# Performance work log

Hardware: AMD Instinct MI355X
Metric: run time of the kernel (lower is better)

## Reference

```python
import jax, jax.numpy as jnp
import numpy as np

N_USER = 60000
N_ITEM = 40000
N = N_USER + N_ITEM          # total nodes
D = 64                        # embed_size
E_HALF = 400000               # undirected interactions; E = 2*E_HALF symmetric directed edges
N_LAYERS = 3                  # len(args.layer_size)
BETA = 0.5                    # self.beta_
EPS = 1e-8                    # torch cosine_similarity eps


def setup_inputs() -> dict:
    key = jax.random.key(0)
    ks = jax.random.split(key, 8)
    # symmetric bipartite edge list: (u, n_user+i) and its reverse
    u = jax.random.randint(ks[0], (E_HALF,), 0, N_USER)
    it = jax.random.randint(ks[1], (E_HALF,), 0, N_ITEM) + N_USER
    src = jnp.concatenate([u, it])
    dst = jnp.concatenate([it, u])
    # rev_perm[e] gives the index of edge (dst[e], src[e])
    rev_perm = jnp.concatenate([jnp.arange(E_HALF) + E_HALF, jnp.arange(E_HALF)])
    vals_half = jax.random.uniform(ks[2], (E_HALF,), minval=0.01, maxval=0.1)
    adj_vals = jnp.concatenate([vals_half, vals_half])  # symmetric normalized adjacency values
    user_emb = 0.1 * jax.random.normal(ks[3], (N_USER, D), dtype=jnp.float32)
    item_emb = 0.1 * jax.random.normal(ks[4], (N_ITEM, D), dtype=jnp.float32)
    W_prune = jax.random.normal(ks[5], (1, 2), dtype=jnp.float32) / jnp.sqrt(2.0)
    b_prune = jnp.zeros((1,), dtype=jnp.float32)
    users = jax.random.randint(ks[6], (2048,), 0, N_USER)
    items = jax.random.randint(ks[7], (2048,), 0, N_ITEM)
    return {"users": users, "items": items, "user_emb": user_emb, "item_emb": item_emb,
            "W_prune": W_prune, "b_prune": b_prune, "src": src, "dst": dst,
            "rev_perm": rev_perm, "adj_vals": adj_vals}


def _computer(user_emb, item_emb, W_prune, b_prune, adj_vals, src, dst, rev_perm):
    emb = jnp.concatenate([user_emb, item_emb], axis=0)  # [N, D]
    embs = [emb]
    mem = adj_vals                                        # memory = adj values at start
    for _ in range(N_LAYERS):
        es, ed = emb[src], emb[dst]                       # [E, D] edge gathers
        # per-edge cosine similarity (torch eps clamp on denominator)
        num = jnp.sum(es * ed, axis=-1)
        den = jnp.maximum(jnp.linalg.norm(es, axis=-1) * jnp.linalg.norm(ed, axis=-1), EPS)
        cos = num / den
        # row-wise L1 normalization over adjacency nonzeros (sklearn normalize, norm='l1')
        rowsum = jax.ops.segment_sum(jnp.abs(cos), src, num_segments=N)
        denom = rowsum[src]
        coef = cos / jnp.where(denom > 0, denom, 1.0)
        # pruning: Linear(2,1) on [coef[r,c], coef[c,r]], sigmoid, keep iff > 0.5
        cv = jnp.stack([coef, coef[rev_perm]], axis=-1)   # [E, 2]
        p = jax.nn.sigmoid(cv @ W_prune.T + b_prune)[:, 0]
        decision = (p > 0.5).astype(coef.dtype)
        coef = coef * decision
        # memory EMA, then elementwise multiply with adjacency -> propagation weights
        mem = BETA * mem + (1.0 - BETA) * coef
        g = mem * adj_vals
        # sparse matmul: out[r] = sum_c A[r,c] * emb[c]
        emb = jax.ops.segment_sum(g[:, None] * ed, src, num_segments=N)
        embs.append(emb)
    light_out = jnp.mean(jnp.stack(embs, axis=1), axis=1)  # [N, D]
    return light_out[:N_USER], light_out[N_USER:]


def reference(users, items, user_emb, item_emb, W_prune, b_prune, src, dst, rev_perm, adj_vals):
    all_users, all_items = _computer(user_emb, item_emb, W_prune, b_prune, adj_vals, src, dst, rev_perm)
    users_emb = all_users[users]                          # [Bu, D]
    items_emb = all_items[items]                          # [Bi, D]
    return jax.nn.sigmoid(users_emb @ items_emb.T)        # [Bu, Bi]
```

## Files before the change

### kernel.cpp

```cpp
#include <hip/hip_runtime.h>
#include <math.h>


#define DD 64
typedef unsigned int u32;

__device__ __forceinline__ float bflo(u32 u) { return __uint_as_float(u << 16); }
__device__ __forceinline__ float bfhi(u32 u) { return __uint_as_float(u & 0xFFFF0000u); }
__device__ __forceinline__ u32 bfpk(float lo, float hi) {
    u32 a = __float_as_uint(lo), b = __float_as_uint(hi);
    a = (a + 0x7FFFu + ((a >> 16) & 1u)) >> 16;
    b = (b + 0x7FFFu + ((b >> 16) & 1u)) & 0xFFFF0000u;
    return a | b;
}
__device__ __forceinline__ void unp16(uint4 q0, uint4 q1, float* f) {
    f[0]=bflo(q0.x); f[1]=bfhi(q0.x); f[2]=bflo(q0.y); f[3]=bfhi(q0.y);
    f[4]=bflo(q0.z); f[5]=bfhi(q0.z); f[6]=bflo(q0.w); f[7]=bfhi(q0.w);
    f[8]=bflo(q1.x); f[9]=bfhi(q1.x); f[10]=bflo(q1.y); f[11]=bfhi(q1.y);
    f[12]=bflo(q1.z); f[13]=bfhi(q1.z); f[14]=bflo(q1.w); f[15]=bfhi(q1.w);
}


__global__ __launch_bounds__(256) void hist_k(const int* __restrict__ src,
                                              int* __restrict__ deg,
                                              int* __restrict__ rank, int E) {
    int e = blockIdx.x * blockDim.x + threadIdx.x;
    if (e < E) rank[e] = atomicAdd(&deg[src[e]], 1);
}

__global__ __launch_bounds__(256) void scan1_k(const int* __restrict__ in,
                                               int* __restrict__ out,
                                               int* __restrict__ partial, int M) {
    __shared__ int sh[256];
    int base = blockIdx.x * 1024;
    int t = threadIdx.x;
    int i0 = base + t * 4;
    int v0 = (i0 + 0 < M) ? in[i0 + 0] : 0;
    int v1 = (i0 + 1 < M) ? in[i0 + 1] : 0;
    int v2 = (i0 + 2 < M) ? in[i0 + 2] : 0;
    int v3 = (i0 + 3 < M) ? in[i0 + 3] : 0;
    int tsum = v0 + v1 + v2 + v3;
    sh[t] = tsum;
    __syncthreads();
    for (int off = 1; off < 256; off <<= 1) {
        int x = (t >= off) ? sh[t - off] : 0;
        __syncthreads();
        sh[t] += x;
        __syncthreads();
    }
    int texcl = sh[t] - tsum;
    if (i0 + 0 < M) out[i0 + 0] = texcl;
    if (i0 + 1 < M) out[i0 + 1] = texcl + v0;
    if (i0 + 2 < M) out[i0 + 2] = texcl + v0 + v1;
    if (i0 + 3 < M) out[i0 + 3] = texcl + v0 + v1 + v2;
    if (t == 255) partial[blockIdx.x] = sh[255];
}

__global__ __launch_bounds__(256) void scan2_k(int* __restrict__ partial, int nc) {
    __shared__ int sh[256];
    int t = threadIdx.x;
    int v = (t < nc) ? partial[t] : 0;
    sh[t] = v;
    __syncthreads();
    for (int off = 1; off < 256; off <<= 1) {
        int x = (t >= off) ? sh[t - off] : 0;
        __syncthreads();
        sh[t] += x;
        __syncthreads();
    }
    if (t < nc) partial[t] = sh[t] - v;
}

__global__ __launch_bounds__(256) void scan3_k(int* __restrict__ out,
                                               const int* __restrict__ partial, int M) {
    int i = blockIdx.x * blockDim.x + threadIdx.x;
    if (i < M) out[i] += partial[i >> 10];
}

__global__ __launch_bounds__(256) void scatter_k(const int* __restrict__ src,
                                                 const int* __restrict__ dst,
                                                 const float* __restrict__ adj,
                                                 const int* __restrict__ rp,
                                                 const int* __restrict__ rank,
                                                 int2* __restrict__ ent,
                                                 int* __restrict__ cidx, int EH) {
    int e = blockIdx.x * blockDim.x + threadIdx.x;
    if (e >= EH) return;
    int u = src[e], i = dst[e];
    int ab = __float_as_int(adj[e]);
    int posU = rp[u] + rank[e];
    int posI = rp[i] + rank[e + EH];
    ent[posU] = make_int2(i, ab);
    ent[posI] = make_int2(u, ab);
    cidx[posI - EH] = posU;
}


__global__ __launch_bounds__(256) void cvt_k(const float* __restrict__ ue,
                                             const float* __restrict__ ie,
                                             u32* __restrict__ tab, int NU, int Nn) {
    int idx = blockIdx.x * blockDim.x + threadIdx.x;
    if (idx >= Nn * 32) return;
    int node = idx >> 5, po = idx & 31;
    const float2* srow = (node < NU) ? (const float2*)(ue + (size_t)node * DD)
                                     : (const float2*)(ie + (size_t)(node - NU) * DD);
    float2 f = srow[po];
    tab[idx] = bfpk(f.x, f.y);
}


__global__ __launch_bounds__(256) void node_norms_k(const u32* __restrict__ tab,
                                                    float* __restrict__ norms, int n) {
    int quad = (blockIdx.x * blockDim.x + threadIdx.x) >> 2;
    int l4   = threadIdx.x & 3;
    if (quad >= n) return;
    const uint4* p = (const uint4*)(tab + (size_t)quad * 32 + l4 * 8);
    float f[16];
    unp16(p[0], p[1], f);
    float s = 0.f;
#pragma unroll
    for (int i = 0; i < 16; ++i) s += f[i] * f[i];
    s += __shfl_xor(s, 1, 64);
    s += __shfl_xor(s, 2, 64);
    if (l4 == 0) norms[quad] = sqrtf(s);
}

__global__ __launch_bounds__(256) void cos_row_k(const u32* __restrict__ tab,
                                                 const float* __restrict__ norms,
                                                 const int* __restrict__ rp,
                                                 const int2* __restrict__ ent,
                                                 float* __restrict__ cosc,
                                                 float* __restrict__ rowsum, int NU) {
    int quad = (blockIdx.x * blockDim.x + threadIdx.x) >> 2;
    int l4   = threadIdx.x & 3;
    if (quad >= NU) return;
    int r  = quad;
    int p0 = rp[r], p1 = rp[r + 1];
    const uint4* ap = (const uint4*)(tab + (size_t)r * 32 + l4 * 8);
    float A[16];
    unp16(ap[0], ap[1], A);
    float nr = norms[r];
    float rs = 0.f;
    int p = p0;
    for (; p + 4 <= p1; p += 4) {
        int d0 = ent[p].x, d1 = ent[p+1].x, d2 = ent[p+2].x, d3 = ent[p+3].x;
        const uint4* q0 = (const uint4*)(tab + (size_t)d0 * 32 + l4 * 8);
        const uint4* q1 = (const uint4*)(tab + (size_t)d1 * 32 + l4 * 8);
        const uint4* q2 = (const uint4*)(tab + (size_t)d2 * 32 + l4 * 8);
        const uint4* q3 = (const uint4*)(tab + (size_t)d3 * 32 + l4 * 8);
        uint4 b00 = q0[0], b01 = q0[1];
        uint4 b10 = q1[0], b11 = q1[1];
        uint4 b20 = q2[0], b21 = q2[1];
        uint4 b30 = q3[0], b31 = q3[1];
        float n0 = norms[d0], n1 = norms[d1], n2 = norms[d2], n3 = norms[d3];
        float B[16];
        float dt0 = 0.f, dt1 = 0.f, dt2 = 0.f, dt3 = 0.f;
        unp16(b00, b01, B);
#pragma unroll
        for (int i = 0; i < 16; ++i) dt0 += A[i] * B[i];
        unp16(b10, b11, B);
#pragma unroll
        for (int i = 0; i < 16; ++i) dt1 += A[i] * B[i];
        unp16(b20, b21, B);
#pragma unroll
        for (int i = 0; i < 16; ++i) dt2 += A[i] * B[i];
        unp16(b30, b31, B);
#pragma unroll
        for (int i = 0; i < 16; ++i) dt3 += A[i] * B[i];
        dt0 += __shfl_xor(dt0, 1, 64); dt0 += __shfl_xor(dt0, 2, 64);
        dt1 += __shfl_xor(dt1, 1, 64); dt1 += __shfl_xor(dt1, 2, 64);
        dt2 += __shfl_xor(dt2, 1, 64); dt2 += __shfl_xor(dt2, 2, 64);
        dt3 += __shfl_xor(dt3, 1, 64); dt3 += __shfl_xor(dt3, 2, 64);
        float c0 = dt0 / fmaxf(nr * n0, 1e-8f);
        float c1 = dt1 / fmaxf(nr * n1, 1e-8f);
        float c2 = dt2 / fmaxf(nr * n2, 1e-8f);
        float c3 = dt3 / fmaxf(nr * n3, 1e-8f);
        if (l4 == 0) {
            cosc[p]   = c0; atomicAdd(&rowsum[d0], fabsf(c0));
            cosc[p+1] = c1; atomicAdd(&rowsum[d1], fabsf(c1));
            cosc[p+2] = c2; atomicAdd(&rowsum[d2], fabsf(c2));
            cosc[p+3] = c3; atomicAdd(&rowsum[d3], fabsf(c3));
        }
        rs += fabsf(c0) + fabsf(c1) + fabsf(c2) + fabsf(c3);
    }
    for (; p < p1; ++p) {
        int d = ent[p].x;
        const uint4* q = (const uint4*)(tab + (size_t)d * 32 + l4 * 8);
        uint4 b0 = q[0], b1 = q[1];
        float B[16];
        unp16(b0, b1, B);
        float dot = 0.f;
#pragma unroll
        for (int i = 0; i < 16; ++i) dot += A[i] * B[i];
        dot += __shfl_xor(dot, 1, 64);
        dot += __shfl_xor(dot, 2, 64);
        float c = dot / fmaxf(nr * norms[d], 1e-8f);
        if (l4 == 0) {
            cosc[p] = c;
            atomicAdd(&rowsum[d], fabsf(c));
        }
        rs += fabsf(c);
    }
    if (l4 == 0) rowsum[r] = rs;
}

__global__ __launch_bounds__(256) void spmm_fused_k(const u32* __restrict__ tab,
                                                    const int* __restrict__ rp,
                                                    const int2* __restrict__ ent,
                                                    const int* __restrict__ cidx,
                                                    const float* __restrict__ cosc,
                                                    const float* __restrict__ rowsum,
                                                    const float* __restrict__ Wp,
                                                    const float* __restrict__ bp,
                                                    float* __restrict__ memc, int useAdj,
                                                    u32* __restrict__ outtab,
                                                    int NU, int EH, int N) {
    int quad = (blockIdx.x * blockDim.x + threadIdx.x) >> 2;
    int l4   = threadIdx.x & 3;
    if (quad >= N) return;
    int r  = quad;
    int p0 = rp[r], p1 = rp[r + 1];
    bool isU = (r < NU);
    float w0 = Wp[0], w1 = Wp[1], bb = bp[0];
    float rs  = rowsum[r];
    float rsg = rs > 0.f ? rs : 1.f;
    float a16[16];
#pragma unroll
    for (int i = 0; i < 16; ++i) a16[i] = 0.f;
    int p = p0;
    for (; p + 4 <= p1; p += 4) {
        int2 t0 = ent[p], t1 = ent[p+1], t2 = ent[p+2], t3 = ent[p+3];
        int c0i = isU ? p   : cidx[p   - EH];
        int c1i = isU ? p+1 : cidx[p+1 - EH];
        int c2i = isU ? p+2 : cidx[p+2 - EH];
        int c3i = isU ? p+3 : cidx[p+3 - EH];
        const uint4* q0 = (const uint4*)(tab + (size_t)t0.x * 32 + l4 * 8);
        const uint4* q1 = (const uint4*)(tab + (size_t)t1.x * 32 + l4 * 8);
        const uint4* q2 = (const uint4*)(tab + (size_t)t2.x * 32 + l4 * 8);
        const uint4* q3 = (const uint4*)(tab + (size_t)t3.x * 32 + l4 * 8);
        uint4 b00 = q0[0], b01 = q0[1];
        uint4 b10 = q1[0], b11 = q1[1];
        uint4 b20 = q2[0], b21 = q2[1];
        uint4 b30 = q3[0], b31 = q3[1];
        float cv0 = cosc[c0i], cv1 = cosc[c1i], cv2 = cosc[c2i], cv3 = cosc[c3i];
        float rd0 = rowsum[t0.x], rd1 = rowsum[t1.x];
        float rd2 = rowsum[t2.x], rd3 = rowsum[t3.x];
        float mp0 = useAdj ? __int_as_float(t0.y) : memc[p];
        float mp1 = useAdj ? __int_as_float(t1.y) : memc[p+1];
        float mp2 = useAdj ? __int_as_float(t2.y) : memc[p+2];
        float mp3 = useAdj ? __int_as_float(t3.y) : memc[p+3];
        float B[16];
#define EDGE(cv, rd, mp, ty, bA, bB, pp)                                    \
        {                                                                   \
            float a = __int_as_float(ty);                                   \
            float rdg = rd > 0.f ? rd : 1.f;                                \
            float c  = cv / rsg;                                            \
            float cr = cv / rdg;                                            \
            float z  = w0 * c + w1 * cr + bb;                               \
            float kept = (z > 0.f) ? c : 0.f;                               \
            float m = 0.5f * mp + 0.5f * kept;                              \
            if (l4 == 0) memc[pp] = m;                                      \
            float g = m * a;                                                \
            unp16(bA, bB, B);                                               \
            _Pragma("unroll")                                               \
            for (int i = 0; i < 16; ++i) a16[i] += g * B[i];                \
        }
        EDGE(cv0, rd0, mp0, t0.y, b00, b01, p)
        EDGE(cv1, rd1, mp1, t1.y, b10, b11, p+1)
        EDGE(cv2, rd2, mp2, t2.y, b20, b21, p+2)
        EDGE(cv3, rd3, mp3, t3.y, b30, b31, p+3)
    }
    for (; p < p1; ++p) {
        int2 t = ent[p];
        int ci = isU ? p : cidx[p - EH];
        const uint4* q = (const uint4*)(tab + (size_t)t.x * 32 + l4 * 8);
        uint4 b0 = q[0], b1 = q[1];
        float cv = cosc[ci];
        float rd = rowsum[t.x];
        float mp = useAdj ? __int_as_float(t.y) : memc[p];
        float B[16];
        EDGE(cv, rd, mp, t.y, b0, b1, p)
    }
#undef EDGE
    uint4 o0, o1;
    o0.x = bfpk(a16[0], a16[1]);   o0.y = bfpk(a16[2], a16[3]);
    o0.z = bfpk(a16[4], a16[5]);   o0.w = bfpk(a16[6], a16[7]);
    o1.x = bfpk(a16[8], a16[9]);   o1.y = bfpk(a16[10], a16[11]);
    o1.z = bfpk(a16[12], a16[13]); o1.w = bfpk(a16[14], a16[15]);
    uint4* op = (uint4*)(outtab + (size_t)r * 32 + l4 * 8);
    op[0] = o0;
    op[1] = o1;
}

__global__ __launch_bounds__(256) void sel_spmm_k(const u32* __restrict__ tab,
                                                  const int* __restrict__ rp,
                                                  const int2* __restrict__ ent,
                                                  const int* __restrict__ cidx,
                                                  const float* __restrict__ cosc,
                                                  const float* __restrict__ rowsum,
                                                  const float* __restrict__ Wp,
                                                  const float* __restrict__ bp,
                                                  const float* __restrict__ memc,
                                                  const int* __restrict__ users,
                                                  const int* __restrict__ items,
                                                  float* __restrict__ acc,
                                                  int BU, int BI, int NU, int EH) {
    int quad = (blockIdx.x * blockDim.x + threadIdx.x) >> 2;
    int l4   = threadIdx.x & 3;
    if (quad >= BU + BI) return;
    int r  = (quad < BU) ? users[quad] : (NU + items[quad - BU]);
    int p0 = rp[r], p1 = rp[r + 1];
    bool isU = (r < NU);
    float w0 = Wp[0], w1 = Wp[1], bb = bp[0];
    float rs  = rowsum[r];
    float rsg = rs > 0.f ? rs : 1.f;
    float a16[16];
#pragma unroll
    for (int i = 0; i < 16; ++i) a16[i] = 0.f;
    int p = p0;
    for (; p + 4 <= p1; p += 4) {
        int2 t0 = ent[p], t1 = ent[p+1], t2 = ent[p+2], t3 = ent[p+3];
        int c0i = isU ? p   : cidx[p   - EH];
        int c1i = isU ? p+1 : cidx[p+1 - EH];
        int c2i = isU ? p+2 : cidx[p+2 - EH];
        int c3i = isU ? p+3 : cidx[p+3 - EH];
        const uint4* q0 = (const uint4*)(tab + (size_t)t0.x * 32 + l4 * 8);
        const uint4* q1 = (const uint4*)(tab + (size_t)t1.x * 32 + l4 * 8);
        const uint4* q2 = (const uint4*)(tab + (size_t)t2.x * 32 + l4 * 8);
        const uint4* q3 = (const uint4*)(tab + (size_t)t3.x * 32 + l4 * 8);
        uint4 b00 = q0[0], b01 = q0[1];
        uint4 b10 = q1[0], b11 = q1[1];
        uint4 b20 = q2[0], b21 = q2[1];
        uint4 b30 = q3[0], b31 = q3[1];
        float cv0 = cosc[c0i], cv1 = cosc[c1i], cv2 = cosc[c2i], cv3 = cosc[c3i];
        float rd0 = rowsum[t0.x], rd1 = rowsum[t1.x];
        float rd2 = rowsum[t2.x], rd3 = rowsum[t3.x];
        float mm0 = memc[p], mm1 = memc[p+1], mm2 = memc[p+2], mm3 = memc[p+3];
        float B[16];
#define EDGES(cv, rd, mm, ty, bA, bB)                                       \
        {                                                                   \
            float a = __int_as_float(ty);                                   \
            float rdg = rd > 0.f ? rd : 1.f;                                \
            float c  = cv / rsg;                                            \
            float cr = cv / rdg;                                            \
            float z  = w0 * c + w1 * cr + bb;                               \
            float kept = (z > 0.f) ? c : 0.f;                               \
            float m = 0.5f * mm + 0.5f * kept;                              \
            float g = m * a;                                                \
            unp16(bA, bB, B);                                               \
            _Pragma("unroll")                                               \
            for (int i = 0; i < 16; ++i) a16[i] += g * B[i];                \
        }
        EDGES(cv0, rd0, mm0, t0.y, b00, b01)
        EDGES(cv1, rd1, mm1, t1.y, b10, b11)
        EDGES(cv2, rd2, mm2, t2.y, b20, b21)
        EDGES(cv3, rd3, mm3, t3.y, b30, b31)
    }
    for (; p < p1; ++p) {
        int2 t = ent[p];
        int ci = isU ? p : cidx[p - EH];
        const uint4* q = (const uint4*)(tab + (size_t)t.x * 32 + l4 * 8);
        uint4 b0 = q[0], b1 = q[1];
        float cv = cosc[ci];
        float rd = rowsum[t.x];
        float mm = memc[p];
        float B[16];
        EDGES(cv, rd, mm, t.y, b0, b1)
    }
#undef EDGES
    float4* av = (float4*)acc;
#pragma unroll
    for (int k = 0; k < 4; ++k) {
        float4 o = av[(size_t)quad * 16 + l4 * 4 + k];
        o.x += a16[k * 4 + 0]; o.y += a16[k * 4 + 1];
        o.z += a16[k * 4 + 2]; o.w += a16[k * 4 + 3];
        av[(size_t)quad * 16 + l4 * 4 + k] = o;
    }
}


__global__ __launch_bounds__(256) void acc_init_k(const float* __restrict__ ue,
                                                  const float* __restrict__ ie,
                                                  const int* __restrict__ users,
                                                  const int* __restrict__ items,
                                                  float* __restrict__ acc,
                                                  int BU, int BI, int NU) {
    int quad = (blockIdx.x * blockDim.x + threadIdx.x) >> 2;
    int l4   = threadIdx.x & 3;
    if (quad >= BU + BI) return;
    int node = (quad < BU) ? users[quad] : (NU + items[quad - BU]);
    const float4* srow = (node < NU) ? (const float4*)(ue + (size_t)node * DD)
                                     : (const float4*)(ie + (size_t)(node - NU) * DD);
    float4* av = (float4*)acc;
#pragma unroll
    for (int k = 0; k < 4; ++k)
        av[(size_t)quad * 16 + l4 * 4 + k] = srow[l4 * 4 + k];
}

__global__ __launch_bounds__(256) void acc_upd_k(const u32* __restrict__ tab,
                                                 const int* __restrict__ users,
                                                 const int* __restrict__ items,
                                                 float* __restrict__ acc,
                                                 int BU, int BI, int NU) {
    int quad = (blockIdx.x * blockDim.x + threadIdx.x) >> 2;
    int l4   = threadIdx.x & 3;
    if (quad >= BU + BI) return;
    int node = (quad < BU) ? users[quad] : (NU + items[quad - BU]);
    const uint4* p = (const uint4*)(tab + (size_t)node * 32 + l4 * 8);
    float f[16];
    unp16(p[0], p[1], f);
    float4* av = (float4*)acc;
#pragma unroll
    for (int k = 0; k < 4; ++k) {
        float4 o = av[(size_t)quad * 16 + l4 * 4 + k];
        o.x += f[k * 4 + 0]; o.y += f[k * 4 + 1];
        o.z += f[k * 4 + 2]; o.w += f[k * 4 + 3];
        av[(size_t)quad * 16 + l4 * 4 + k] = o;
    }
}

__global__ __launch_bounds__(256) void final_gemm_k(const float* __restrict__ acc,
                                                    float* __restrict__ out,
                                                    int BU, int BI) {
    __shared__ float Us[64][65];
    __shared__ float Is[64][65];
    int t = threadIdx.x;
    int i0 = blockIdx.y * 64, j0 = blockIdx.x * 64;
#pragma unroll
    for (int i = 0; i < 4; ++i) {
        int f4 = t + i * 256;
        int r = f4 >> 4, c4 = (f4 & 15) * 4;
        float4 u4 = *(const float4*)&acc[(size_t)(i0 + r) * DD + c4];
        float4 v4 = *(const float4*)&acc[(size_t)(BU + j0 + r) * DD + c4];
        Us[r][c4 + 0] = u4.x; Us[r][c4 + 1] = u4.y;
        Us[r][c4 + 2] = u4.z; Us[r][c4 + 3] = u4.w;
        Is[r][c4 + 0] = v4.x; Is[r][c4 + 1] = v4.y;
        Is[r][c4 + 2] = v4.z; Is[r][c4 + 3] = v4.w;
    }
    __syncthreads();
    int tx = t & 15, ty = t >> 4;
    float s[4][4];
#pragma unroll
    for (int i = 0; i < 4; ++i)
#pragma unroll
        for (int j = 0; j < 4; ++j) s[i][j] = 0.f;
    for (int k = 0; k < 64; ++k) {
        float u[4], v[4];
#pragma unroll
        for (int i = 0; i < 4; ++i) u[i] = Us[ty * 4 + i][k];
#pragma unroll
        for (int j = 0; j < 4; ++j) v[j] = Is[tx * 4 + j][k];
#pragma unroll
        for (int i = 0; i < 4; ++i)
#pragma unroll
            for (int j = 0; j < 4; ++j) s[i][j] += u[i] * v[j];
    }
#pragma unroll
    for (int i = 0; i < 4; ++i) {
        float4 o;
        o.x = 1.f / (1.f + expf(-s[i][0] * 0.0625f));
        o.y = 1.f / (1.f + expf(-s[i][1] * 0.0625f));
        o.z = 1.f / (1.f + expf(-s[i][2] * 0.0625f));
        o.w = 1.f / (1.f + expf(-s[i][3] * 0.0625f));
        *(float4*)&out[(size_t)(i0 + ty * 4 + i) * BI + j0 + tx * 4] = o;
    }
}


extern "C" void kernel_launch(void* const* d_in, const int* in_sizes, int n_in,
                              void* d_out, int out_size, void* d_ws, size_t ws_size,
                              hipStream_t stream) {
    const int*   users    = (const int*)d_in[0];
    const int*   items    = (const int*)d_in[1];
    const float* user_emb = (const float*)d_in[2];
    const float* item_emb = (const float*)d_in[3];
    const float* Wp       = (const float*)d_in[4];
    const float* bp       = (const float*)d_in[5];
    const int*   src      = (const int*)d_in[6];
    const int*   dst      = (const int*)d_in[7];
    const float* adj      = (const float*)d_in[9];

    int BU = in_sizes[0];
    int BI = in_sizes[1];
    int NU = in_sizes[2] / DD;
    int NI = in_sizes[3] / DD;
    int Nn = NU + NI;
    int E  = in_sizes[6];
    int EH = E / 2;
    int M  = Nn + 1;
    int Mp = (M + 3) & ~3;

    u32*   tabA   = (u32*)d_ws;
    u32*   tabB   = tabA + (size_t)Nn * 32;
    int2*  ent    = (int2*)(tabB + (size_t)Nn * 32);
    int*   cidx   = (int*)(ent + E);
    float* norms  = (float*)(cidx + EH);
    float* rowsum = norms + Nn;
    float* cosc   = rowsum + Nn;
    float* memc   = cosc + EH;
    float* acc    = memc + E;
    int*   deg    = (int*)(acc + (size_t)(BU + BI) * DD);
    int*   rp     = deg + Mp;
    int*   rank   = rp + Mp;
    int*   partial= rank + E;

    int eb  = (E + 255) / 256;
    int ehb = (EH + 255) / 256;
    int nc  = (M + 1023) / 1024;

    hipMemsetAsync(deg, 0, sizeof(int) * (size_t)M, stream);
    hist_k<<<eb, 256, 0, stream>>>(src, deg, rank, E);
    scan1_k<<<nc, 256, 0, stream>>>(deg, rp, partial, M);
    scan2_k<<<1, 256, 0, stream>>>(partial, nc);
    scan3_k<<<(M + 255) / 256, 256, 0, stream>>>(rp, partial, M);
    scatter_k<<<ehb, 256, 0, stream>>>(src, dst, adj, rp, rank, ent, cidx, EH);

    cvt_k<<<(Nn * 32 + 255) / 256, 256, 0, stream>>>(user_emb, item_emb, tabA, NU, Nn);
    int selBlocks = (4 * (BU + BI) + 255) / 256;
    acc_init_k<<<selBlocks, 256, 0, stream>>>(user_emb, item_emb, users, items, acc,
                                              BU, BI, NU);

    int rowBlocksU = (4 * NU + 255) / 256;
    int rowBlocksN = (4 * Nn + 255) / 256;
    u32* cur = tabA;
    u32* nxt = tabB;
    for (int layer = 0; layer < 3; ++layer) {
        hipMemsetAsync(rowsum + NU, 0, sizeof(float) * (size_t)NI, stream);
        node_norms_k<<<rowBlocksN, 256, 0, stream>>>(cur, norms, Nn);
        cos_row_k<<<rowBlocksU, 256, 0, stream>>>(cur, norms, rp, ent, cosc, rowsum, NU);
        if (layer < 2) {
            spmm_fused_k<<<rowBlocksN, 256, 0, stream>>>(cur, rp, ent, cidx, cosc,
                                                         rowsum, Wp, bp, memc,
                                                         layer == 0 ? 1 : 0, nxt,
                                                         NU, EH, Nn);
            acc_upd_k<<<selBlocks, 256, 0, stream>>>(nxt, users, items, acc, BU, BI, NU);
            u32* t = cur; cur = nxt; nxt = t;
        } else {
            sel_spmm_k<<<selBlocks, 256, 0, stream>>>(cur, rp, ent, cidx, cosc, rowsum,
                                                      Wp, bp, memc, users, items,
                                                      acc, BU, BI, NU, EH);
        }
    }

    dim3 grid(BI / 64, BU / 64);
    final_gemm_k<<<grid, 256, 0, stream>>>(acc, (float*)d_out, BU, BI);
}
```

Baseline: 358.7 us.

## Fuse norms, rowsum zeroing and acc updates into neighboring kernels to cut launches

Node norm computation moves into the producer kernels: the conversion kernel computes norms from the bf16-rounded values, and the SpMM kernel computes norms of its output rows. Rowsum zeroing now happens inside those kernels, using double-buffered rowsum arrays instead of per-layer memsets. The acc init and update work rides along as extra blocks of the conversion and cosine kernels. This removes several launches and a full re-read of the embedding table per layer. Norms in SpMM come from the fp32 accumulators rather than the rounded bf16 values, which can slightly change numerics.

```diff
diff --git a/kernel.cpp b/kernel.cpp
--- a/kernel.cpp
+++ b/kernel.cpp
@@ -96,45 +96,98 @@
 }
 
 
-__global__ __launch_bounds__(256) void cvt_k(const float* __restrict__ ue,
-                                             const float* __restrict__ ie,
-                                             u32* __restrict__ tab, int NU, int Nn) {
-    int idx = blockIdx.x * blockDim.x + threadIdx.x;
-    if (idx >= Nn * 32) return;
-    int node = idx >> 5, po = idx & 31;
-    const float2* srow = (node < NU) ? (const float2*)(ue + (size_t)node * DD)
-                                     : (const float2*)(ie + (size_t)(node - NU) * DD);
-    float2 f = srow[po];
-    tab[idx] = bfpk(f.x, f.y);
-}
-
-
-__global__ __launch_bounds__(256) void node_norms_k(const u32* __restrict__ tab,
-                                                    float* __restrict__ norms, int n) {
-    int quad = (blockIdx.x * blockDim.x + threadIdx.x) >> 2;
-    int l4   = threadIdx.x & 3;
-    if (quad >= n) return;
-    const uint4* p = (const uint4*)(tab + (size_t)quad * 32 + l4 * 8);
-    float f[16];
-    unp16(p[0], p[1], f);
-    float s = 0.f;
-#pragma unroll
-    for (int i = 0; i < 16; ++i) s += f[i] * f[i];
-    s += __shfl_xor(s, 1, 64);
-    s += __shfl_xor(s, 2, 64);
-    if (l4 == 0) norms[quad] = sqrtf(s);
-}
-
-__global__ __launch_bounds__(256) void cos_row_k(const u32* __restrict__ tab,
+__global__ __launch_bounds__(256) void cvt_fused_k(const float* __restrict__ ue,
+                                                   const float* __restrict__ ie,
+                                                   const int* __restrict__ users,
+                                                   const int* __restrict__ items,
+                                                   u32* __restrict__ tab,
+                                                   float* __restrict__ norms,
+                                                   float* __restrict__ rsA,
+                                                   float* __restrict__ acc,
+                                                   int NU, int Nn, int BU, int BI,
+                                                   int cvtBlocks) {
+    int b = blockIdx.x;
+    if (b < cvtBlocks) {
+        int x = b * 256 + threadIdx.x;
+        if (x >= Nn * 4) return;
+        int node = x >> 2, l4 = x & 3;
+        const float4* srow = (node < NU)
+            ? (const float4*)(ue + (size_t)node * DD)
+            : (const float4*)(ie + (size_t)(node - NU) * DD);
+        float f[16];
+#pragma unroll
+        for (int k = 0; k < 4; ++k) {
+            float4 v = srow[l4 * 4 + k];
+            f[k*4+0] = v.x; f[k*4+1] = v.y; f[k*4+2] = v.z; f[k*4+3] = v.w;
+        }
+        uint4 o0, o1;
+        o0.x = bfpk(f[0], f[1]);   o0.y = bfpk(f[2], f[3]);
+        o0.z = bfpk(f[4], f[5]);   o0.w = bfpk(f[6], f[7]);
+        o1.x = bfpk(f[8], f[9]);   o1.y = bfpk(f[10], f[11]);
+        o1.z = bfpk(f[12], f[13]); o1.w = bfpk(f[14], f[15]);
+        uint4* op = (uint4*)(tab + (size_t)node * 32 + l4 * 8);
+        op[0] = o0;
+        op[1] = o1;
+        float fb[16];
+        unp16(o0, o1, fb);
+        float s = 0.f;
+#pragma unroll
+        for (int i = 0; i < 16; ++i) s += fb[i] * fb[i];
+        s += __shfl_xor(s, 1, 64);
+        s += __shfl_xor(s, 2, 64);
+        if (l4 == 0) {
+            norms[node] = sqrtf(s);
+            if (node >= NU) rsA[node] = 0.f;
+        }
+    } else {
+        int x = (b - cvtBlocks) * 256 + threadIdx.x;
+        if (x >= (BU + BI) * 4) return;
+        int q_ = x >> 2, l4 = x & 3;
+        int node = (q_ < BU) ? users[q_] : (NU + items[q_ - BU]);
+        const float4* srow = (node < NU)
+            ? (const float4*)(ue + (size_t)node * DD)
+            : (const float4*)(ie + (size_t)(node - NU) * DD);
+        float4* av = (float4*)acc;
+#pragma unroll
+        for (int k = 0; k < 4; ++k)
+            av[(size_t)q_ * 16 + l4 * 4 + k] = srow[l4 * 4 + k];
+    }
+}
+
+
+__global__ __launch_bounds__(256) void cos_acc_k(const u32* __restrict__ tab,
                                                  const float* __restrict__ norms,
                                                  const int* __restrict__ rp,
                                                  const int2* __restrict__ ent,
                                                  float* __restrict__ cosc,
-                                                 float* __restrict__ rowsum, int NU) {
-    int quad = (blockIdx.x * blockDim.x + threadIdx.x) >> 2;
-    int l4   = threadIdx.x & 3;
-    if (quad >= NU) return;
-    int r  = quad;
+                                                 float* __restrict__ rowsum,
+                                                 const int* __restrict__ users,
+                                                 const int* __restrict__ items,
+                                                 float* __restrict__ acc,
+                                                 int NU, int BU, int BI,
+                                                 int cosBlocks) {
+    int b = blockIdx.x;
+    if (b >= cosBlocks) {
+        int x = (b - cosBlocks) * 256 + threadIdx.x;
+        if (x >= (BU + BI) * 4) return;
+        int q_ = x >> 2, l4 = x & 3;
+        int node = (q_ < BU) ? users[q_] : (NU + items[q_ - BU]);
+        const uint4* p = (const uint4*)(tab + (size_t)node * 32 + l4 * 8);
+        float f[16];
+        unp16(p[0], p[1], f);
+        float4* av = (float4*)acc;
+#pragma unroll
+        for (int k = 0; k < 4; ++k) {
+            float4 o = av[(size_t)q_ * 16 + l4 * 4 + k];
+            o.x += f[k * 4 + 0]; o.y += f[k * 4 + 1];
+            o.z += f[k * 4 + 2]; o.w += f[k * 4 + 3];
+            av[(size_t)q_ * 16 + l4 * 4 + k] = o;
+        }
+        return;
+    }
+    int x = b * 256 + threadIdx.x;
+    if (x >= NU * 4) return;
+    int r = x >> 2, l4 = x & 3;
     int p0 = rp[r], p1 = rp[r + 1];
     const uint4* ap = (const uint4*)(tab + (size_t)r * 32 + l4 * 8);
     float A[16];
@@ -204,6 +257,7 @@
     if (l4 == 0) rowsum[r] = rs;
 }
 
+
 __global__ __launch_bounds__(256) void spmm_fused_k(const u32* __restrict__ tab,
                                                     const int* __restrict__ rp,
                                                     const int2* __restrict__ ent,
@@ -214,11 +268,12 @@
                                                     const float* __restrict__ bp,
                                                     float* __restrict__ memc, int useAdj,
                                                     u32* __restrict__ outtab,
+                                                    float* __restrict__ norms,
+                                                    float* __restrict__ rsnext,
                                                     int NU, int EH, int N) {
-    int quad = (blockIdx.x * blockDim.x + threadIdx.x) >> 2;
-    int l4   = threadIdx.x & 3;
-    if (quad >= N) return;
-    int r  = quad;
+    int x = blockIdx.x * 256 + threadIdx.x;
+    if (x >= N * 4) return;
+    int r = x >> 2, l4 = x & 3;
     int p0 = rp[r], p1 = rp[r + 1];
     bool isU = (r < NU);
     float w0 = Wp[0], w1 = Wp[1], bb = bp[0];
@@ -282,6 +337,15 @@
         EDGE(cv, rd, mp, t.y, b0, b1, p)
     }
 #undef EDGE
+    float s = 0.f;
+#pragma unroll
+    for (int i = 0; i < 16; ++i) s += a16[i] * a16[i];
+    s += __shfl_xor(s, 1, 64);
+    s += __shfl_xor(s, 2, 64);
+    if (l4 == 0) {
+        norms[r] = sqrtf(s);
+        if (r >= NU) rsnext[r] = 0.f;
+    }
     uint4 o0, o1;
     o0.x = bfpk(a16[0], a16[1]);   o0.y = bfpk(a16[2], a16[3]);
     o0.z = bfpk(a16[4], a16[5]);   o0.w = bfpk(a16[6], a16[7]);
@@ -291,6 +355,7 @@
     op[0] = o0;
     op[1] = o1;
 }
+
 
 __global__ __launch_bounds__(256) void sel_spmm_k(const u32* __restrict__ tab,
                                                   const int* __restrict__ rp,
@@ -305,10 +370,10 @@
                                                   const int* __restrict__ items,
                                                   float* __restrict__ acc,
                                                   int BU, int BI, int NU, int EH) {
-    int quad = (blockIdx.x * blockDim.x + threadIdx.x) >> 2;
-    int l4   = threadIdx.x & 3;
-    if (quad >= BU + BI) return;
-    int r  = (quad < BU) ? users[quad] : (NU + items[quad - BU]);
+    int x = blockIdx.x * 256 + threadIdx.x;
+    if (x >= (BU + BI) * 4) return;
+    int q_ = x >> 2, l4 = x & 3;
+    int r = (q_ < BU) ? users[q_] : (NU + items[q_ - BU]);
     int p0 = rp[r], p1 = rp[r + 1];
     bool isU = (r < NU);
     float w0 = Wp[0], w1 = Wp[1], bb = bp[0];
@@ -371,53 +436,13 @@
     float4* av = (float4*)acc;
 #pragma unroll
     for (int k = 0; k < 4; ++k) {
-        float4 o = av[(size_t)quad * 16 + l4 * 4 + k];
+        float4 o = av[(size_t)q_ * 16 + l4 * 4 + k];
         o.x += a16[k * 4 + 0]; o.y += a16[k * 4 + 1];
         o.z += a16[k * 4 + 2]; o.w += a16[k * 4 + 3];
-        av[(size_t)quad * 16 + l4 * 4 + k] = o;
-    }
-}
-
-
-__global__ __launch_bounds__(256) void acc_init_k(const float* __restrict__ ue,
-                                                  const float* __restrict__ ie,
-                                                  const int* __restrict__ users,
-                                                  const int* __restrict__ items,
-                                                  float* __restrict__ acc,
-                                                  int BU, int BI, int NU) {
-    int quad = (blockIdx.x * blockDim.x + threadIdx.x) >> 2;
-    int l4   = threadIdx.x & 3;
-    if (quad >= BU + BI) return;
-    int node = (quad < BU) ? users[quad] : (NU + items[quad - BU]);
-    const float4* srow = (node < NU) ? (const float4*)(ue + (size_t)node * DD)
-                                     : (const float4*)(ie + (size_t)(node - NU) * DD);
-    float4* av = (float4*)acc;
-#pragma unroll
-    for (int k = 0; k < 4; ++k)
-        av[(size_t)quad * 16 + l4 * 4 + k] = srow[l4 * 4 + k];
-}
-
-__global__ __launch_bounds__(256) void acc_upd_k(const u32* __restrict__ tab,
-                                                 const int* __restrict__ users,
-                                                 const int* __restrict__ items,
-                                                 float* __restrict__ acc,
-                                                 int BU, int BI, int NU) {
-    int quad = (blockIdx.x * blockDim.x + threadIdx.x) >> 2;
-    int l4   = threadIdx.x & 3;
-    if (quad >= BU + BI) return;
-    int node = (quad < BU) ? users[quad] : (NU + items[quad - BU]);
-    const uint4* p = (const uint4*)(tab + (size_t)node * 32 + l4 * 8);
-    float f[16];
-    unp16(p[0], p[1], f);
-    float4* av = (float4*)acc;
-#pragma unroll
-    for (int k = 0; k < 4; ++k) {
-        float4 o = av[(size_t)quad * 16 + l4 * 4 + k];
-        o.x += f[k * 4 + 0]; o.y += f[k * 4 + 1];
-        o.z += f[k * 4 + 2]; o.w += f[k * 4 + 3];
-        av[(size_t)quad * 16 + l4 * 4 + k] = o;
-    }
-}
+        av[(size_t)q_ * 16 + l4 * 4 + k] = o;
+    }
+}
+
 
 __global__ __launch_bounds__(256) void final_gemm_k(const float* __restrict__ acc,
                                                     float* __restrict__ out,
@@ -495,8 +520,9 @@
     int2*  ent    = (int2*)(tabB + (size_t)Nn * 32);
     int*   cidx   = (int*)(ent + E);
     float* norms  = (float*)(cidx + EH);
-    float* rowsum = norms + Nn;
-    float* cosc   = rowsum + Nn;
+    float* rsA    = norms + Nn;
+    float* rsB    = rsA + Nn;
+    float* cosc   = rsB + Nn;
     float* memc   = cosc + EH;
     float* acc    = memc + E;
     int*   deg    = (int*)(acc + (size_t)(BU + BI) * DD);
@@ -515,32 +541,29 @@
     scan3_k<<<(M + 255) / 256, 256, 0, stream>>>(rp, partial, M);
     scatter_k<<<ehb, 256, 0, stream>>>(src, dst, adj, rp, rank, ent, cidx, EH);
 
-    cvt_k<<<(Nn * 32 + 255) / 256, 256, 0, stream>>>(user_emb, item_emb, tabA, NU, Nn);
-    int selBlocks = (4 * (BU + BI) + 255) / 256;
-    acc_init_k<<<selBlocks, 256, 0, stream>>>(user_emb, item_emb, users, items, acc,
-                                              BU, BI, NU);
-
-    int rowBlocksU = (4 * NU + 255) / 256;
-    int rowBlocksN = (4 * Nn + 255) / 256;
-    u32* cur = tabA;
-    u32* nxt = tabB;
-    for (int layer = 0; layer < 3; ++layer) {
-        hipMemsetAsync(rowsum + NU, 0, sizeof(float) * (size_t)NI, stream);
-        node_norms_k<<<rowBlocksN, 256, 0, stream>>>(cur, norms, Nn);
-        cos_row_k<<<rowBlocksU, 256, 0, stream>>>(cur, norms, rp, ent, cosc, rowsum, NU);
-        if (layer < 2) {
-            spmm_fused_k<<<rowBlocksN, 256, 0, stream>>>(cur, rp, ent, cidx, cosc,
-                                                         rowsum, Wp, bp, memc,
-                                                         layer == 0 ? 1 : 0, nxt,
-                                                         NU, EH, Nn);
-            acc_upd_k<<<selBlocks, 256, 0, stream>>>(nxt, users, items, acc, BU, BI, NU);
-            u32* t = cur; cur = nxt; nxt = t;
-        } else {
-            sel_spmm_k<<<selBlocks, 256, 0, stream>>>(cur, rp, ent, cidx, cosc, rowsum,
-                                                      Wp, bp, memc, users, items,
-                                                      acc, BU, BI, NU, EH);
-        }
-    }
+    int cvtBlocks = (Nn * 4 + 255) / 256;
+    int selBlocks = ((BU + BI) * 4 + 255) / 256;
+    cvt_fused_k<<<cvtBlocks + selBlocks, 256, 0, stream>>>(user_emb, item_emb, users,
+                                                           items, tabA, norms, rsA, acc,
+                                                           NU, Nn, BU, BI, cvtBlocks);
+
+    int cosBlocks = (NU * 4 + 255) / 256;
+    int nBlocks   = (Nn * 4 + 255) / 256;
+
+    cos_acc_k<<<cosBlocks, 256, 0, stream>>>(tabA, norms, rp, ent, cosc, rsA,
+                                             users, items, acc, NU, BU, BI, cosBlocks);
+    spmm_fused_k<<<nBlocks, 256, 0, stream>>>(tabA, rp, ent, cidx, cosc, rsA, Wp, bp,
+                                              memc, 1, tabB, norms, rsB, NU, EH, Nn);
+    cos_acc_k<<<cosBlocks + selBlocks, 256, 0, stream>>>(tabB, norms, rp, ent, cosc, rsB,
+                                                         users, items, acc, NU, BU, BI,
+                                                         cosBlocks);
+    spmm_fused_k<<<nBlocks, 256, 0, stream>>>(tabB, rp, ent, cidx, cosc, rsB, Wp, bp,
+                                              memc, 0, tabA, norms, rsA, NU, EH, Nn);
+    cos_acc_k<<<cosBlocks + selBlocks, 256, 0, stream>>>(tabA, norms, rp, ent, cosc, rsA,
+                                                         users, items, acc, NU, BU, BI,
+                                                         cosBlocks);
+    sel_spmm_k<<<selBlocks, 256, 0, stream>>>(tabA, rp, ent, cidx, cosc, rsA, Wp, bp,
+                                              memc, users, items, acc, BU, BI, NU, EH);
 
     dim3 grid(BI / 64, BU / 64);
     final_gemm_k<<<grid, 256, 0, stream>>>(acc, (float*)d_out, BU, BI);
```

Measured after the change: 342.4 us. 4.5% less time.
